# Kernel tuning notes

Measured on AMD Instinct MI355X. Metric: run time of the kernel, lower is better.

The kernel has to match this reference:

```python
import jax, jax.numpy as jnp
import numpy as np

D_MODEL = 1024
N_HEADS = 16
HEAD_DIM = D_MODEL // N_HEADS
NEG_INF = -1e10


def setup_inputs() -> dict:
    key = jax.random.key(0)
    ks = jax.random.split(key, 6)
    B, S = 2, 2048
    x = jax.random.normal(ks[0], (B, S, D_MODEL), dtype=jnp.float32)
    mask = jnp.ones((B, S), dtype=jnp.int32)
    scale_w = 1.0 / np.sqrt(D_MODEL)
    Wq = jax.random.normal(ks[1], (D_MODEL, D_MODEL), dtype=jnp.float32) * scale_w
    Wk = jax.random.normal(ks[2], (D_MODEL, D_MODEL), dtype=jnp.float32) * scale_w
    Wv = jax.random.normal(ks[3], (D_MODEL, D_MODEL), dtype=jnp.float32) * scale_w
    Wo = jax.random.normal(ks[4], (D_MODEL, D_MODEL), dtype=jnp.float32) * scale_w
    bq = jnp.zeros((D_MODEL,), jnp.float32)
    bk = jnp.zeros((D_MODEL,), jnp.float32)
    bv = jnp.zeros((D_MODEL,), jnp.float32)
    bo = jnp.zeros((D_MODEL,), jnp.float32)
    return {"x": x, "mask": mask, "Wq": Wq, "bq": bq, "Wk": Wk, "bk": bk,
            "Wv": Wv, "bv": bv, "Wo": Wo, "bo": bo}


def reference(x, mask, Wq, bq, Wk, bk, Wv, bv, Wo, bo):
    B, S, _ = x.shape
    # Linear projections (torch Linear: y = x @ W.T + b)
    Q = x @ Wq.T + bq
    K = x @ Wk.T + bk
    V = x @ Wv.T + bv
    # [B, H, S, Dh]
    Q = Q.reshape(B, S, N_HEADS, HEAD_DIM).transpose(0, 2, 1, 3)
    K = K.reshape(B, S, N_HEADS, HEAD_DIM).transpose(0, 2, 1, 3)
    V = V.reshape(B, S, N_HEADS, HEAD_DIM).transpose(0, 2, 1, 3)
    scale = jnp.sqrt(jnp.float32(HEAD_DIM))
    energy = jnp.einsum('bhqd,bhkd->bhqk', Q, K) / scale  # [B,H,S,S]
    # mask: [B,S] -> broadcast over heads and query dim (keys masked)
    m = mask[:, None, None, :]  # [B,1,1,S]
    energy = jnp.where(m == 0, jnp.float32(NEG_INF), energy)
    attention = jax.nn.softmax(energy, axis=-1)
    # dropout in eval mode = identity
    out = jnp.einsum('bhqk,bhkd->bhqd', attention, V)  # [B,H,S,Dh]
    out = out.transpose(0, 2, 1, 3).reshape(B, S, D_MODEL)
    return out @ Wo.T + bo
```

## Files before the change

### kernel.cpp

```cpp
#include <hip/hip_runtime.h>
#include <hip/hip_bf16.h>

typedef __hip_bfloat16 bf16;
typedef __attribute__((ext_vector_type(8))) short s8v;
typedef __attribute__((ext_vector_type(4))) float f4v;

#define D_MODEL 1024
#define S_LEN   2048
#define BATCH   2
#define NH      16
#define HD      64
#define M_TOTAL 4096
#define NT      (S_LEN / 64)

__device__ __forceinline__ void gll16(const bf16* g, bf16* l) {
    __builtin_amdgcn_global_load_lds(
        (const __attribute__((address_space(1))) void*)g,
        (__attribute__((address_space(3))) void*)l, 16, 0, 0);
}

struct CvtPtrs {
    const float* sx; bf16* dx;
    const float* s0; const float* s1; const float* s2; const float* s3;
    bf16* d0; bf16* d1; bf16* d2; bf16* d3;
};

__global__ __launch_bounds__(256) void cvt_all(CvtPtrs p) {
    const int bid = blockIdx.x;
    const float* s; bf16* d; int i;
    if (bid < 2048) {
        s = p.sx; d = p.dx;
        i = (bid * 256 + threadIdx.x) * 8;
    } else {
        const int wsel = (bid - 2048) >> 9;
        const int wb   = (bid - 2048) & 511;
        s = (wsel == 0) ? p.s0 : (wsel == 1) ? p.s1 : (wsel == 2) ? p.s2 : p.s3;
        d = (wsel == 0) ? p.d0 : (wsel == 1) ? p.d1 : (wsel == 2) ? p.d2 : p.d3;
        i = (wb * 256 + threadIdx.x) * 8;
    }
    float4 a = *(const float4*)(s + i);
    float4 b = *(const float4*)(s + i + 4);
    union { bf16 h[8]; uint4 u; } q;
    q.h[0] = __float2bfloat16(a.x); q.h[1] = __float2bfloat16(a.y);
    q.h[2] = __float2bfloat16(a.z); q.h[3] = __float2bfloat16(a.w);
    q.h[4] = __float2bfloat16(b.x); q.h[5] = __float2bfloat16(b.y);
    q.h[6] = __float2bfloat16(b.z); q.h[7] = __float2bfloat16(b.w);
    *(uint4*)(d + i) = q.u;
}

template<int TM, int TN>
__device__ __forceinline__ void gemm_main(const bf16* __restrict__ A,
                                          const bf16* __restrict__ W,
                                          bf16* As, bf16* Bs,
                                          int bm, int bn,
                                          f4v (&acc)[TM/32][TN/32])
{
    constexpr int FM = TM / 32, FN = TN / 32;
    constexpr int CALLS_A = TM / 16, CALLS = (TM + TN) / 16, PW = CALLS / 4;
    const int t = threadIdx.x, wv = t >> 6, lane = t & 63;
    const int quad = lane >> 4, l15 = lane & 15;
    const int wm = (wv >> 1) * (TM / 2), wn = (wv & 1) * (TN / 2);
    const int lr = lane >> 2, lc = (lane & 3) * 8;

    auto STAGE = [&](int buf, int k0) {
        #pragma unroll
        for (int c = 0; c < PW; ++c) {
            const int cc = wv * PW + c;
            if (cc < CALLS_A) {
                gll16(A + (size_t)(bm + cc * 16 + lr) * D_MODEL + k0 + lc,
                      As + buf * (TM * 32) + cc * 16 * 32);
            } else {
                const int r2 = cc - CALLS_A;
                gll16(W + (size_t)(bn + r2 * 16 + lr) * D_MODEL + k0 + lc,
                      Bs + buf * (TN * 32) + r2 * 16 * 32);
            }
        }
    };

    STAGE(0, 0);
    __syncthreads();
    int cur = 0;

    for (int k0 = 0; k0 < D_MODEL; k0 += 32) {
        if (k0 + 32 < D_MODEL) STAGE(cur ^ 1, k0 + 32);

        const bf16* ab = As + cur * (TM * 32);
        const bf16* bb = Bs + cur * (TN * 32);
        s8v af[FM], bfv[FN];
        #pragma unroll
        for (int i = 0; i < FM; ++i)
            af[i] = *(const s8v*)(ab + (wm + i * 16 + l15) * 32 + quad * 8);
        #pragma unroll
        for (int j = 0; j < FN; ++j)
            bfv[j] = *(const s8v*)(bb + (wn + j * 16 + l15) * 32 + quad * 8);
        __builtin_amdgcn_s_setprio(1);
        #pragma unroll
        for (int i = 0; i < FM; ++i)
            #pragma unroll
            for (int j = 0; j < FN; ++j)
                acc[i][j] = __builtin_amdgcn_mfma_f32_16x16x32_bf16(af[i], bfv[j], acc[i][j], 0, 0, 0);
        __builtin_amdgcn_s_setprio(0);

        __syncthreads();
        cur ^= 1;
    }
}

__global__ __launch_bounds__(256) void gemm_qkv(
    const bf16* __restrict__ x,
    const bf16* __restrict__ Wq, const bf16* __restrict__ Wk, const bf16* __restrict__ Wv,
    const float* __restrict__ bq, const float* __restrict__ bk, const float* __restrict__ bv,
    bf16* __restrict__ Qb, bf16* __restrict__ Kb, bf16* __restrict__ Vtb)
{
    __shared__ __align__(16) char smem[4 * 64 * 72 * 2];
    bf16* As = (bf16*)smem;
    bf16* Bs = (bf16*)(smem + 2 * 128 * 32 * 2);
    bf16 (*Tw)[64][72] = (bf16(*)[64][72])smem;

    const int z = blockIdx.z;
    const bf16*  W    = (z == 0) ? Wq : (z == 1) ? Wk : Wv;
    const float* bias = (z == 0) ? bq : (z == 1) ? bk : bv;
    bf16*        out  = (z == 0) ? Qb : (z == 1) ? Kb : Vtb;
    const int bm = blockIdx.y * 128, bn = blockIdx.x * 128;

    f4v acc[4][4] = {};
    gemm_main<128, 128>(x, W, As, Bs, bm, bn, acc);

    const int t = threadIdx.x, wv = t >> 6, lane = t & 63;
    const int quad = lane >> 4, l15 = lane & 15;
    const int wm = (wv >> 1) * 64, wn = (wv & 1) * 64;

    if (z == 2) {
        __syncthreads();
        #pragma unroll
        for (int j = 0; j < 4; ++j) {
            const int col = bn + wn + j * 16 + l15;
            const float bv_ = bias[col];
            #pragma unroll
            for (int i = 0; i < 4; ++i) {
                #pragma unroll
                for (int rp = 0; rp < 4; rp += 2) {
                    union { bf16 h[2]; unsigned u; } p2;
                    p2.h[0] = __float2bfloat16(acc[i][j][rp]     + bv_);
                    p2.h[1] = __float2bfloat16(acc[i][j][rp + 1] + bv_);
                    *(unsigned*)&Tw[wv][j * 16 + l15][i * 16 + quad * 4 + rp] = p2.u;
                }
            }
        }
        const int bb = (bm + wm) >> 11, s0 = (bm + wm) & 2047;
        #pragma unroll
        for (int p = 0; p < 8; ++p) {
            const int dl = p * 8 + (lane >> 3);
            const int sl = (lane & 7) * 8;
            const int col = bn + wn + dl;
            const int h = col >> 6, d = col & 63;
            uint4 v = *(const uint4*)&Tw[wv][dl][sl];
            *(uint4*)&out[(((size_t)(bb * NH + h)) * HD + d) * S_LEN + s0 + sl] = v;
        }
    } else {
        #pragma unroll
        for (int j = 0; j < 4; ++j) {
            const int col = bn + wn + j * 16 + l15;
            const float bv_ = bias[col];
            const int h = col >> 6, d = col & 63;
            #pragma unroll
            for (int i = 0; i < 4; ++i) {
                #pragma unroll
                for (int r = 0; r < 4; ++r) {
                    const int row = bm + wm + i * 16 + quad * 4 + r;
                    const int b = row >> 11, s = row & 2047;
                    const float v = acc[i][j][r] + bv_;
                    out[(((size_t)(b * NH + h)) * S_LEN + s) * HD + d] = __float2bfloat16(v);
                }
            }
        }
    }
}

__global__ __launch_bounds__(256) void gemm_out(
    const bf16* __restrict__ Ob, const bf16* __restrict__ Wo,
    const float* __restrict__ bo, float* __restrict__ out)
{
    __shared__ __align__(16) bf16 As[2][64 * 32];
    __shared__ __align__(16) bf16 Bs[2][128 * 32];
    const int bm = blockIdx.y * 64, bn = blockIdx.x * 128;

    f4v acc[2][4] = {};
    gemm_main<64, 128>(Ob, Wo, &As[0][0], &Bs[0][0], bm, bn, acc);

    const int t = threadIdx.x, wv = t >> 6, lane = t & 63;
    const int quad = lane >> 4, l15 = lane & 15;
    const int wm = (wv >> 1) * 32, wn = (wv & 1) * 64;
    #pragma unroll
    for (int j = 0; j < 4; ++j) {
        const int col = bn + wn + j * 16 + l15;
        const float bv_ = bo[col];
        #pragma unroll
        for (int i = 0; i < 2; ++i)
            #pragma unroll
            for (int r = 0; r < 4; ++r) {
                const int row = bm + wm + i * 16 + quad * 4 + r;
                out[(size_t)row * D_MODEL + col] = acc[i][j][r] + bv_;
            }
    }
}

__global__ __launch_bounds__(256) void attn_mfma(
    const bf16* __restrict__ Q, const bf16* __restrict__ K,
    const bf16* __restrict__ Vt, const int* __restrict__ mask,
    bf16* __restrict__ O)
{
    __shared__ __align__(16) bf16 Ks[2][64][64];
    __shared__ __align__(16) bf16 Vts[2][64][64];
    __shared__ __align__(16) bf16 Ps[4][16][64];

    const int t = threadIdx.x, wv = t >> 6, lane = t & 63;
    const int quad = lane >> 4, l15 = lane & 15;
    const int sw = l15 & 7;
    const int bid = blockIdx.x;
    const int qt = bid & 31, h = (bid >> 5) & 15, b = bid >> 9;
    const int q0 = qt * 64;
    const size_t qkbase = ((size_t)(b * NH + h)) * S_LEN * HD;
    const size_t vtbase = ((size_t)(b * NH + h)) * HD * S_LEN;

    const float KSC  = 0.125f * 1.44269504f;
    const float THR2 = 8.0f * 1.44269504f;

    const bf16* qrow = Q + qkbase + (size_t)(q0 + wv * 16 + l15) * HD;
    const s8v qf0 = *(const s8v*)(qrow + quad * 8);
    const s8v qf1 = *(const s8v*)(qrow + 32 + quad * 8);

    const int srow = t >> 2;
    const int swr  = srow & 7;
    const int c2   = (t & 3) * 2;
    const int ch0  = c2 ^ swr, ch1 = (c2 + 1) ^ swr;

    uint4 kr0, kr1, vr0, vr1;
    auto LOADT = [&](int kt2) {
        const int kk = kt2 * 64;
        const uint4* kp = (const uint4*)(K  + qkbase + (size_t)(kk + srow) * HD + c2 * 8);
        const uint4* vp = (const uint4*)(Vt + vtbase + (size_t)srow * S_LEN + kk + c2 * 8);
        kr0 = kp[0]; kr1 = kp[1];
        vr0 = vp[0]; vr1 = vp[1];
    };
    auto STAGE = [&](int bf) {
        *(uint4*)&Ks[bf][srow][ch0 * 8]  = kr0;
        *(uint4*)&Ks[bf][srow][ch1 * 8]  = kr1;
        *(uint4*)&Vts[bf][srow][ch0 * 8] = vr0;
        *(uint4*)&Vts[bf][srow][ch1 * 8] = vr1;
    };

    LOADT(0);
    STAGE(0);
    __syncthreads();

    float mprev = -1e30f, lsum = 0.f;
    f4v oacc[4] = {};
    int cur = 0;

    for (int kt = 0; kt < NT; ++kt) {
        const int k0 = kt * 64;
        const bool more = (kt + 1 < NT);
        if (more) LOADT(kt + 1);

        const char* kbase = (const char*)&Ks[cur][0][0];
        const char* vbase = (const char*)&Vts[cur][0][0];

        f4v st[4];
        __builtin_amdgcn_s_setprio(1);
        #pragma unroll
        for (int c = 0; c < 4; ++c) {
            const char* kr = kbase + (c * 16 + l15) * 128;
            s8v kf0 = *(const s8v*)(kr + ((quad ^ sw) << 4));
            s8v kf1 = *(const s8v*)(kr + (((4 + quad) ^ sw) << 4));
            f4v z = {0.f, 0.f, 0.f, 0.f};
            z = __builtin_amdgcn_mfma_f32_16x16x32_bf16(kf0, qf0, z, 0, 0, 0);
            z = __builtin_amdgcn_mfma_f32_16x16x32_bf16(kf1, qf1, z, 0, 0, 0);
            st[c] = z;
        }
        __builtin_amdgcn_s_setprio(0);

        float mt = -1e30f;
        #pragma unroll
        for (int c = 0; c < 4; ++c) {
            const int4 mkc = *(const int4*)&mask[b * S_LEN + k0 + c * 16 + quad * 4];
            f4v m4;
            m4[0] = mkc.x ? 0.f : -1e30f;
            m4[1] = mkc.y ? 0.f : -1e30f;
            m4[2] = mkc.z ? 0.f : -1e30f;
            m4[3] = mkc.w ? 0.f : -1e30f;
            st[c] = st[c] * KSC + m4;
            mt = fmaxf(mt, fmaxf(fmaxf(st[c][0], st[c][1]), fmaxf(st[c][2], st[c][3])));
        }
        mt = fmaxf(mt, __shfl_xor(mt, 16, 64));
        mt = fmaxf(mt, __shfl_xor(mt, 32, 64));

        float mn = mprev;
        if (!__all(mt <= mprev + THR2)) {
            mn = fmaxf(mprev, mt);
            const float alpha = __builtin_amdgcn_exp2f(mprev - mn);
            mprev = mn;
            float av[4];
            #pragma unroll
            for (int r = 0; r < 4; ++r) av[r] = __shfl(alpha, quad * 4 + r, 64);
            #pragma unroll
            for (int dt = 0; dt < 4; ++dt)
                #pragma unroll
                for (int r = 0; r < 4; ++r) oacc[dt][r] *= av[r];
            lsum *= alpha;
        }

        f4v psv = {0.f, 0.f, 0.f, 0.f};
        #pragma unroll
        for (int c = 0; c < 4; ++c) {
            f4v e = st[c] - mn;
            e[0] = __builtin_amdgcn_exp2f(e[0]);
            e[1] = __builtin_amdgcn_exp2f(e[1]);
            e[2] = __builtin_amdgcn_exp2f(e[2]);
            e[3] = __builtin_amdgcn_exp2f(e[3]);
            st[c] = e;
            psv += e;
        }
        lsum += psv[0] + psv[1] + psv[2] + psv[3];

        if (more) STAGE(cur ^ 1);

        char* pr = (char*)&Ps[wv][l15][0];
        #pragma unroll
        for (int c = 0; c < 4; ++c) {
            union { bf16 hh[4]; short4 s4; } pk;
            pk.hh[0] = __float2bfloat16(st[c][0]);
            pk.hh[1] = __float2bfloat16(st[c][1]);
            pk.hh[2] = __float2bfloat16(st[c][2]);
            pk.hh[3] = __float2bfloat16(st[c][3]);
            const int wch = (2 * c + (quad >> 1)) ^ sw;
            *(short4*)(pr + (wch << 4) + ((quad & 1) << 3)) = pk.s4;
        }
        s8v pf0 = *(const s8v*)(pr + ((quad ^ sw) << 4));
        s8v pf1 = *(const s8v*)(pr + (((4 + quad) ^ sw) << 4));

        __builtin_amdgcn_s_setprio(1);
        #pragma unroll
        for (int dt = 0; dt < 4; ++dt) {
            const char* vr = vbase + (dt * 16 + l15) * 128;
            s8v vf0 = *(const s8v*)(vr + ((quad ^ sw) << 4));
            s8v vf1 = *(const s8v*)(vr + (((4 + quad) ^ sw) << 4));
            oacc[dt] = __builtin_amdgcn_mfma_f32_16x16x32_bf16(pf0, vf0, oacc[dt], 0, 0, 0);
            oacc[dt] = __builtin_amdgcn_mfma_f32_16x16x32_bf16(pf1, vf1, oacc[dt], 0, 0, 0);
        }
        __builtin_amdgcn_s_setprio(0);

        if (more) __syncthreads();
        cur ^= 1;
    }

    lsum += __shfl_xor(lsum, 16, 64);
    lsum += __shfl_xor(lsum, 32, 64);
    float linv[4];
    #pragma unroll
    for (int r = 0; r < 4; ++r) linv[r] = 1.f / __shfl(lsum, quad * 4 + r, 64);
    #pragma unroll
    for (int dt = 0; dt < 4; ++dt) {
        #pragma unroll
        for (int r = 0; r < 4; ++r) {
            const int s = q0 + wv * 16 + quad * 4 + r;
            const int col = h * 64 + dt * 16 + l15;
            O[((size_t)b * S_LEN + s) * D_MODEL + col] = __float2bfloat16(oacc[dt][r] * linv[r]);
        }
    }
}

extern "C" void kernel_launch(void* const* d_in, const int* in_sizes, int n_in,
                              void* d_out, int out_size, void* d_ws, size_t ws_size,
                              hipStream_t stream) {
    const float* x    = (const float*)d_in[0];
    const int*   mask = (const int*)  d_in[1];
    const float* Wq   = (const float*)d_in[2];
    const float* bq   = (const float*)d_in[3];
    const float* Wk   = (const float*)d_in[4];
    const float* bk   = (const float*)d_in[5];
    const float* Wv   = (const float*)d_in[6];
    const float* bv   = (const float*)d_in[7];
    const float* Wo   = (const float*)d_in[8];
    const float* bo   = (const float*)d_in[9];
    float* out = (float*)d_out;

    char* w = (char*)d_ws;
    bf16* xb  = (bf16*)w; w += (size_t)M_TOTAL * D_MODEL * 2;
    bf16* Wqb = (bf16*)w; w += (size_t)D_MODEL * D_MODEL * 2;
    bf16* Wkb = (bf16*)w; w += (size_t)D_MODEL * D_MODEL * 2;
    bf16* Wvb = (bf16*)w; w += (size_t)D_MODEL * D_MODEL * 2;
    bf16* Wob = (bf16*)w; w += (size_t)D_MODEL * D_MODEL * 2;
    bf16* Qb  = (bf16*)w; w += (size_t)M_TOTAL * D_MODEL * 2;
    bf16* Kb  = (bf16*)w; w += (size_t)M_TOTAL * D_MODEL * 2;
    bf16* Vtb = (bf16*)w; w += (size_t)M_TOTAL * D_MODEL * 2;
    bf16* Ob  = (bf16*)w; w += (size_t)M_TOTAL * D_MODEL * 2;

    CvtPtrs cp = { x, xb, Wq, Wk, Wv, Wo, Wqb, Wkb, Wvb, Wob };
    cvt_all<<<4096, 256, 0, stream>>>(cp);

    gemm_qkv<<<dim3(8, 32, 3), 256, 0, stream>>>(xb, Wqb, Wkb, Wvb, bq, bk, bv, Qb, Kb, Vtb);

    attn_mfma<<<BATCH * NH * (S_LEN / 64), 256, 0, stream>>>(Qb, Kb, Vtb, mask, Ob);

    gemm_out<<<dim3(8, 64), 256, 0, stream>>>(Ob, Wob, bo, out);
}
```

Measured before the change: 241.8 us.

## Load K/V MFMA fragments directly from global into registers, drop LDS staging

```diff
diff --git a/kernel.cpp b/kernel.cpp
--- a/kernel.cpp
+++ b/kernel.cpp
@@ -210,15 +210,13 @@
     const bf16* __restrict__ Vt, const int* __restrict__ mask,
     bf16* __restrict__ O)
 {
-    __shared__ __align__(16) bf16 Ks[2][64][64];
-    __shared__ __align__(16) bf16 Vts[2][64][64];
     __shared__ __align__(16) bf16 Ps[4][16][64];
 
     const int t = threadIdx.x, wv = t >> 6, lane = t & 63;
     const int quad = lane >> 4, l15 = lane & 15;
     const int sw = l15 & 7;
     const int bid = blockIdx.x;
-    const int qt = bid & 31, h = (bid >> 5) & 15, b = bid >> 9;
+    const int b = bid & 1, h = (bid >> 1) & 15, qt = bid >> 5;
     const int q0 = qt * 64;
     const size_t qkbase = ((size_t)(b * NH + h)) * S_LEN * HD;
     const size_t vtbase = ((size_t)(b * NH + h)) * HD * S_LEN;
@@ -230,55 +228,68 @@
     const s8v qf0 = *(const s8v*)(qrow + quad * 8);
     const s8v qf1 = *(const s8v*)(qrow + 32 + quad * 8);
 
-    const int srow = t >> 2;
-    const int swr  = srow & 7;
-    const int c2   = (t & 3) * 2;
-    const int ch0  = c2 ^ swr, ch1 = (c2 + 1) ^ swr;
-
-    uint4 kr0, kr1, vr0, vr1;
-    auto LOADT = [&](int kt2) {
+    const bf16* kf_base = K  + qkbase + (size_t)l15 * HD    + quad * 8;
+    const bf16* vf_base = Vt + vtbase + (size_t)l15 * S_LEN + quad * 8;
+
+    s8v k00, k01, k10, k11, k20, k21, k30, k31;
+    s8v v00, v01, v10, v11, v20, v21, v30, v31;
+
+    auto LOADK = [&](int kt2) {
         const int kk = kt2 * 64;
-        const uint4* kp = (const uint4*)(K  + qkbase + (size_t)(kk + srow) * HD + c2 * 8);
-        const uint4* vp = (const uint4*)(Vt + vtbase + (size_t)srow * S_LEN + kk + c2 * 8);
-        kr0 = kp[0]; kr1 = kp[1];
-        vr0 = vp[0]; vr1 = vp[1];
+        const bf16* p0 = kf_base + (size_t)(kk +  0) * HD;
+        const bf16* p1 = kf_base + (size_t)(kk + 16) * HD;
+        const bf16* p2 = kf_base + (size_t)(kk + 32) * HD;
+        const bf16* p3 = kf_base + (size_t)(kk + 48) * HD;
+        k00 = *(const s8v*)(p0); k01 = *(const s8v*)(p0 + 32);
+        k10 = *(const s8v*)(p1); k11 = *(const s8v*)(p1 + 32);
+        k20 = *(const s8v*)(p2); k21 = *(const s8v*)(p2 + 32);
+        k30 = *(const s8v*)(p3); k31 = *(const s8v*)(p3 + 32);
     };
-    auto STAGE = [&](int bf) {
-        *(uint4*)&Ks[bf][srow][ch0 * 8]  = kr0;
-        *(uint4*)&Ks[bf][srow][ch1 * 8]  = kr1;
-        *(uint4*)&Vts[bf][srow][ch0 * 8] = vr0;
-        *(uint4*)&Vts[bf][srow][ch1 * 8] = vr1;
+    auto LOADV = [&](int kt2) {
+        const int kk = kt2 * 64;
+        const bf16* p0 = vf_base + (size_t)( 0) * S_LEN + kk;
+        const bf16* p1 = vf_base + (size_t)(16) * S_LEN + kk;
+        const bf16* p2 = vf_base + (size_t)(32) * S_LEN + kk;
+        const bf16* p3 = vf_base + (size_t)(48) * S_LEN + kk;
+        v00 = *(const s8v*)(p0); v01 = *(const s8v*)(p0 + 32);
+        v10 = *(const s8v*)(p1); v11 = *(const s8v*)(p1 + 32);
+        v20 = *(const s8v*)(p2); v21 = *(const s8v*)(p2 + 32);
+        v30 = *(const s8v*)(p3); v31 = *(const s8v*)(p3 + 32);
     };
 
-    LOADT(0);
-    STAGE(0);
-    __syncthreads();
+    LOADK(0);
+    LOADV(0);
 
     float mprev = -1e30f, lsum = 0.f;
     f4v oacc[4] = {};
-    int cur = 0;
 
     for (int kt = 0; kt < NT; ++kt) {
         const int k0 = kt * 64;
         const bool more = (kt + 1 < NT);
-        if (more) LOADT(kt + 1);
-
-        const char* kbase = (const char*)&Ks[cur][0][0];
-        const char* vbase = (const char*)&Vts[cur][0][0];
 
         f4v st[4];
         __builtin_amdgcn_s_setprio(1);
-        #pragma unroll
-        for (int c = 0; c < 4; ++c) {
-            const char* kr = kbase + (c * 16 + l15) * 128;
-            s8v kf0 = *(const s8v*)(kr + ((quad ^ sw) << 4));
-            s8v kf1 = *(const s8v*)(kr + (((4 + quad) ^ sw) << 4));
-            f4v z = {0.f, 0.f, 0.f, 0.f};
-            z = __builtin_amdgcn_mfma_f32_16x16x32_bf16(kf0, qf0, z, 0, 0, 0);
-            z = __builtin_amdgcn_mfma_f32_16x16x32_bf16(kf1, qf1, z, 0, 0, 0);
-            st[c] = z;
+        {
+            f4v z0 = {0.f, 0.f, 0.f, 0.f};
+            z0 = __builtin_amdgcn_mfma_f32_16x16x32_bf16(k00, qf0, z0, 0, 0, 0);
+            z0 = __builtin_amdgcn_mfma_f32_16x16x32_bf16(k01, qf1, z0, 0, 0, 0);
+            st[0] = z0;
+            f4v z1 = {0.f, 0.f, 0.f, 0.f};
+            z1 = __builtin_amdgcn_mfma_f32_16x16x32_bf16(k10, qf0, z1, 0, 0, 0);
+            z1 = __builtin_amdgcn_mfma_f32_16x16x32_bf16(k11, qf1, z1, 0, 0, 0);
+            st[1] = z1;
+            f4v z2 = {0.f, 0.f, 0.f, 0.f};
+            z2 = __builtin_amdgcn_mfma_f32_16x16x32_bf16(k20, qf0, z2, 0, 0, 0);
+            z2 = __builtin_amdgcn_mfma_f32_16x16x32_bf16(k21, qf1, z2, 0, 0, 0);
+            st[2] = z2;
+            f4v z3 = {0.f, 0.f, 0.f, 0.f};
+            z3 = __builtin_amdgcn_mfma_f32_16x16x32_bf16(k30, qf0, z3, 0, 0, 0);
+            z3 = __builtin_amdgcn_mfma_f32_16x16x32_bf16(k31, qf1, z3, 0, 0, 0);
+            st[3] = z3;
         }
         __builtin_amdgcn_s_setprio(0);
+
+        if (more) LOADK(kt + 1);
 
         float mt = -1e30f;
         #pragma unroll
@@ -323,8 +334,6 @@
         }
         lsum += psv[0] + psv[1] + psv[2] + psv[3];
 
-        if (more) STAGE(cur ^ 1);
-
         char* pr = (char*)&Ps[wv][l15][0];
         #pragma unroll
         for (int c = 0; c < 4; ++c) {
@@ -340,18 +349,17 @@
         s8v pf1 = *(const s8v*)(pr + (((4 + quad) ^ sw) << 4));
 
         __builtin_amdgcn_s_setprio(1);
-        #pragma unroll
-        for (int dt = 0; dt < 4; ++dt) {
-            const char* vr = vbase + (dt * 16 + l15) * 128;
-            s8v vf0 = *(const s8v*)(vr + ((quad ^ sw) << 4));
-            s8v vf1 = *(const s8v*)(vr + (((4 + quad) ^ sw) << 4));
-            oacc[dt] = __builtin_amdgcn_mfma_f32_16x16x32_bf16(pf0, vf0, oacc[dt], 0, 0, 0);
-            oacc[dt] = __builtin_amdgcn_mfma_f32_16x16x32_bf16(pf1, vf1, oacc[dt], 0, 0, 0);
-        }
+        oacc[0] = __builtin_amdgcn_mfma_f32_16x16x32_bf16(pf0, v00, oacc[0], 0, 0, 0);
+        oacc[0] = __builtin_amdgcn_mfma_f32_16x16x32_bf16(pf1, v01, oacc[0], 0, 0, 0);
+        oacc[1] = __builtin_amdgcn_mfma_f32_16x16x32_bf16(pf0, v10, oacc[1], 0, 0, 0);
+        oacc[1] = __builtin_amdgcn_mfma_f32_16x16x32_bf16(pf1, v11, oacc[1], 0, 0, 0);
+        oacc[2] = __builtin_amdgcn_mfma_f32_16x16x32_bf16(pf0, v20, oacc[2], 0, 0, 0);
+        oacc[2] = __builtin_amdgcn_mfma_f32_16x16x32_bf16(pf1, v21, oacc[2], 0, 0, 0);
+        oacc[3] = __builtin_amdgcn_mfma_f32_16x16x32_bf16(pf0, v30, oacc[3], 0, 0, 0);
+        oacc[3] = __builtin_amdgcn_mfma_f32_16x16x32_bf16(pf1, v31, oacc[3], 0, 0, 0);
         __builtin_amdgcn_s_setprio(0);
 
-        if (more) __syncthreads();
-        cur ^= 1;
+        if (more) LOADV(kt + 1);
     }
 
     lsum += __shfl_xor(lsum, 16, 64);
```

Result: slower. 386.5 us (+59.8%).
